# Optimization experiments

Measured on AMD Instinct MI355X. Metric: run time of the kernel, lower is better.

## Reference

```python
import jax, jax.numpy as jnp
import numpy as np

LATENT = 292
T = 120          # max_length
CHARSET = 35     # charset_length
B = 512
H1, H2, H3 = 701, 701, 901


def _p(key, shape, scale=0.05):
    return jax.random.normal(key, shape, dtype=jnp.float32) * scale


def setup_inputs() -> dict:
    key = jax.random.key(0)
    ks = jax.random.split(key, 12)
    z32 = lambda *s: jnp.zeros(s, jnp.float32)
    return {
        "z": jax.random.normal(ks[0], (B, LATENT), dtype=jnp.float32),
        # linear_1: Dense(latent_dim, selu)
        "W1": _p(ks[1], (LATENT, LATENT)), "b1": z32(LATENT),
        # gru_1 (Keras GRU, reset_after=True): kernel [in,3H], recurrent [H,3H], two bias vectors [3H]
        "gWi1": _p(ks[2], (LATENT, 3 * H1)), "gWh1": _p(ks[3], (H1, 3 * H1)),
        "gbi1": z32(3 * H1), "gbh1": z32(3 * H1),
        # gru_2
        "gWi2": _p(ks[4], (H1, 3 * H2)), "gWh2": _p(ks[5], (H2, 3 * H2)),
        "gbi2": z32(3 * H2), "gbh2": z32(3 * H2),
        # gru_3
        "gWi3": _p(ks[6], (H2, 3 * H3)), "gWh3": _p(ks[7], (H3, 3 * H3)),
        "gbi3": z32(3 * H3), "gbh3": z32(3 * H3),
        # linear_2: TimeDistributed(Dense(charset_length))
        "Wo": _p(ks[8], (H3, CHARSET)), "bo": z32(CHARSET),
    }


def _gru(x_seq, Wi, Wh, bi, bh):
    """Keras GRU (reset_after=True, gate order z,r,h), return_sequences=True.
    x_seq: [B,T,D] -> [B,T,H]. Input projections hoisted out of the scan."""
    H = Wh.shape[0]
    bsz = x_seq.shape[0]
    xp = jnp.einsum('btd,dg->btg', x_seq, Wi) + bi  # [B,T,3H]
    xp = jnp.transpose(xp, (1, 0, 2))               # [T,B,3H] for scan
    h0 = jnp.zeros((bsz, H), x_seq.dtype)

    def step(h, xt):
        rp = h @ Wh + bh                             # recurrent projection [B,3H]
        xz, xr, xh = jnp.split(xt, 3, axis=-1)
        rz, rr, rh = jnp.split(rp, 3, axis=-1)
        zg = jax.nn.sigmoid(xz + rz)
        rg = jax.nn.sigmoid(xr + rr)
        hh = jnp.tanh(xh + rg * rh)                  # reset applied after recurrent matmul
        hn = zg * h + (1.0 - zg) * hh
        return hn, hn

    _, ys = jax.lax.scan(step, h0, xp)               # ys: [T,B,H]
    return jnp.transpose(ys, (1, 0, 2))


def reference(z, W1, b1, gWi1, gWh1, gbi1, gbh1, gWi2, gWh2, gbi2, gbh2,
              gWi3, gWh3, gbi3, gbh3, Wo, bo):
    x = jax.nn.selu(z @ W1 + b1)                             # [B,latent]
    xs = jnp.broadcast_to(x[:, None, :], (x.shape[0], T, x.shape[1]))  # RepeatVector
    h = _gru(xs, gWi1, gWh1, gbi1, gbh1)                     # [B,T,701]
    h = _gru(h, gWi2, gWh2, gbi2, gbh2)                      # [B,T,701] (dropout inactive at inference)
    h = _gru(h, gWi3, gWh3, gbi3, gbh3)                      # [B,T,901]
    logits = jnp.einsum('bth,hc->btc', h, Wo) + bo           # [B,T,charset]
    return jax.nn.softmax(logits, axis=2)
```

## Files before the change

kernel.cpp:

```cpp
#include <hip/hip_runtime.h>
#include <hip/hip_bf16.h>
#include <math.h>

typedef unsigned short u16;
typedef __attribute__((ext_vector_type(4))) float f32x4;
typedef __attribute__((ext_vector_type(8))) short s16x8;

#define BB  512
#define TT  120
#define LAT 292
#define HH1 701
#define HH3 901
#define H1P 704
#define H3P 960
#define CH  35

static const size_t O_X    = 0;
static const size_t O_XP1  = 598016;
static const size_t O_H1F  = 4923392;
static const size_t O_H2F  = 7806976;
static const size_t O_H3F  = 10690560;
static const size_t O_H1B  = 14622720;
static const size_t O_H2B  = 16064512;
static const size_t O_H3B  = 17506304;
static const size_t O_WHT1 = 19472384;
static const size_t O_WIT2 = 22446080;
static const size_t O_WHT2 = 25419776;
static const size_t O_WIT3 = 28393472;
static const size_t O_WHT3 = 32358400;
static const size_t O_WOT  = 37765120;
static const size_t O_TAB  = 37888000;
static const size_t ZERO_BYTES = 14548992;

#define DSWZ(row, g) ((((g) ^ ((row) & 7)) << 4))

static __device__ __forceinline__ u16 f2b(float f){
  union { float f; unsigned int i; } v; v.f = f;
  unsigned int x = v.i;
  return (u16)((x + 0x7FFFu + ((x >> 16) & 1u)) >> 16);
}

#define GLL16(g, l) __builtin_amdgcn_global_load_lds( \
    (const __attribute__((address_space(1))) unsigned int*)(g), \
    (__attribute__((address_space(3))) unsigned int*)(l), 16, 0, 0)

__launch_bounds__(256)
__global__ void k_selu(const float* __restrict__ z, const float* __restrict__ W1,
                       const float* __restrict__ b1, float* __restrict__ x)
{
  int idx = blockIdx.x * 256 + threadIdx.x;
  if (idx >= BB * LAT) return;
  int b = idx / LAT, i = idx - b * LAT;
  float acc = b1[i];
  const float* zr = z + (size_t)b * LAT;
  for (int k = 0; k < LAT; ++k)
    acc += zr[k] * W1[k * LAT + i];
  const float alpha = 1.6732632423543772f, scale = 1.0507009873554805f;
  x[idx] = scale * (acc > 0.f ? acc : alpha * (expf(acc) - 1.f));
}

__launch_bounds__(256)
__global__ void k_xp1(const float* __restrict__ x, const float* __restrict__ Wi1,
                      const float* __restrict__ bi1, float* __restrict__ xp1)
{
  int nb = blockIdx.x % 9, bb = blockIdx.x / 9;
  int n = nb * 256 + threadIdx.x;
  int b0 = bb * 8;
  if (n >= 2112) return;
  if (n >= 2103) { for (int r = 0; r < 8; ++r) xp1[(size_t)(b0 + r) * 2112 + n] = 0.f; return; }
  float bias = bi1[n];
  float acc[8];
  for (int r = 0; r < 8; ++r) acc[r] = bias;
  for (int k = 0; k < LAT; ++k) {
    float w = Wi1[(size_t)k * 2103 + n];
    #pragma unroll
    for (int r = 0; r < 8; ++r) acc[r] += x[(size_t)(b0 + r) * LAT + k] * w;
  }
  for (int r = 0; r < 8; ++r) xp1[(size_t)(b0 + r) * 2112 + n] = acc[r];
}

__launch_bounds__(256)
__global__ void k_transpose(const float* __restrict__ W, u16* __restrict__ WT,
                            int K, int N, int Kpad, int RowsPad)
{
  int tilesN = RowsPad / 64;
  int tk = blockIdx.x / tilesN, tn = blockIdx.x % tilesN;
  int k0 = tk * 64, n0 = tn * 64;
  __shared__ u16 lds[64][72];
  int tid = threadIdx.x;
  int nl = tid & 63, q = tid >> 6;
  for (int i = 0; i < 16; ++i) {
    int kl = q * 16 + i;
    int k = k0 + kl, n = n0 + nl;
    lds[kl][nl] = (k < K && n < N) ? f2b(W[(size_t)k * N + n]) : (u16)0;
  }
  __syncthreads();
  for (int i = 0; i < 16; ++i) {
    int rl = q * 16 + i;
    WT[(size_t)(n0 + rl) * Kpad + k0 + nl] = lds[nl][rl];
  }
}

__global__ void k_maketab(unsigned int* __restrict__ tab)
{
  if (threadIdx.x != 0 || blockIdx.x != 0) return;
  for (int x = 0; x < 8; ++x) {
    for (int li = 0; li < 32; ++li) {
      unsigned v;
      if (li < 15) {
        int t3 = 15 * x + li;
        v = 0xFFFF0000u | (2u << 12) | ((unsigned)(t3 & 7) << 8) | (unsigned)(t3 >> 3);
      } else if (li < 26) {
        int t2 = 11 * x + (li - 15);
        v = 0xFFFF0000u | (1u << 12) | ((unsigned)(t2 & 7) << 8) | (unsigned)(t2 >> 3);
      } else if (li < 31) {
        int pi = 5 * x + (li - 26);
        int i0 = 2 * pi, i1 = 2 * pi + 1;
        unsigned lo = ((unsigned)(i0 & 7) << 8) | (unsigned)(i0 >> 3);
        unsigned hw = ((unsigned)(i1 & 7) << 8) | (unsigned)(i1 >> 3);
        v = lo | (hw << 16);
      } else {
        if (x < 4) {
          unsigned lo = (3u << 12) | ((unsigned)(2 * x) << 8);
          unsigned hw = (3u << 12) | ((unsigned)(2 * x + 1) << 8);
          v = lo | (hw << 16);
        } else {
          int pi = 40 + (x - 4);
          int i0 = 2 * pi, i1 = 2 * pi + 1;
          unsigned lo = ((unsigned)(i0 & 7) << 8) | (unsigned)(i0 >> 3);
          unsigned hw = ((unsigned)(i1 & 7) << 8) | (unsigned)(i1 >> 3);
          v = lo | (hw << 16);
        }
      }
      tab[x + 8 * li] = v;
    }
  }
}

#define RD32(base, row, q) ((base) + (row) * 64 + ((((q) - ((row) >> 2)) & 3) << 4))

static __device__ __forceinline__ void stage32(
    const u16* __restrict__ A, int As, const u16* __restrict__ W, int Ws, int WH,
    int r0, int j0, int kbase, int wl, int lane, char* buf)
{
  #pragma unroll
  for (int i = 0; i < 4; ++i) {
    const int si = wl * 4 + i;
    char* l = buf + si * 1024;
    if (si < 4) {
      int slot = si * 64 + lane;
      int row = slot >> 2, gl = slot & 3;
      int gq = (gl + (row >> 2)) & 3;
      GLL16(A + (size_t)(r0 + row) * As + kbase + gq * 8, l);
    } else {
      int s2 = si * 64 + lane - 256;
      int gate = s2 >> 8, loc = s2 & 255;
      int col = loc >> 2, gl = loc & 3;
      int gq = (gl + (col >> 2)) & 3;
      GLL16(W + ((size_t)gate * WH + j0 + col) * Ws + kbase + gq * 8, l);
    }
  }
}

template<int HACC>
static __device__ __forceinline__ void mm32(const char* gb, int wr, int wc, int m16, int kg,
                                            f32x4 (&acc)[4][2][2])
{
  s16x8 af[2];
  #pragma unroll
  for (int fm = 0; fm < 2; ++fm) {
    int row = wr * 32 + fm * 16 + m16;
    af[fm] = *(const s16x8*)RD32(gb, row, kg);
  }
  #pragma unroll
  for (int g = 0; g < 3; ++g) {
    #pragma unroll
    for (int fn = 0; fn < 2; ++fn) {
      int col = wc * 32 + fn * 16 + m16;
      s16x8 bf = *(const s16x8*)RD32(gb + 4096 + g * 4096, col, kg);
      const int ai = (g == 2) ? HACC : g;
      #pragma unroll
      for (int fm = 0; fm < 2; ++fm)
        acc[ai][fm][fn] = __builtin_amdgcn_mfma_f32_16x16x32_bf16(af[fm], bf, acc[ai][fm][fn], 0, 0, 0);
    }
  }
}

static __device__ __forceinline__ void gru_pipe32(
    const u16* A0, int As0, const u16* W0, int Ws0,
    const u16* A1, int As1, const u16* W1p, int Ws1,
    int WH, int n0, int n1, int k1off,
    int r0, int j0, char* ring, int wl, int lane,
    int wr, int wc, int m16, int kg, f32x4 (&acc)[4][2][2])
{
  const int n = n0 + n1;
#define STG32(C) do { int c_ = (C); char* b_ = ring + (c_ & 3) * 16384; \
    if (c_ < n0) stage32(A0, As0, W0, Ws0, WH, r0, j0, c_ * 32, wl, lane, b_); \
    else         stage32(A1, As1, W1p, Ws1, WH, r0, j0, (c_ - n0) * 32 + k1off, wl, lane, b_); \
  } while (0)
  STG32(0); STG32(1); STG32(2);
  for (int ch = 0; ch < n; ++ch) {
    if (ch + 2 < n)      asm volatile("s_waitcnt vmcnt(8)" ::: "memory");
    else if (ch + 1 < n) asm volatile("s_waitcnt vmcnt(4)" ::: "memory");
    else                 asm volatile("s_waitcnt vmcnt(0)" ::: "memory");
    __builtin_amdgcn_s_barrier();
    if (ch + 3 < n) STG32(ch + 3);
    if (ch < n0) mm32<2>(ring + (ch & 3) * 16384, wr, wc, m16, kg, acc);
    else         mm32<3>(ring + (ch & 3) * 16384, wr, wc, m16, kg, acc);
  }
#undef STG32
}

__launch_bounds__(512, 2)
__global__ void k_wave(int s, const unsigned int* __restrict__ tab,
    const u16* __restrict__ WhT1, const u16* __restrict__ WiT2, const u16* __restrict__ WhT2,
    const u16* __restrict__ WiT3, const u16* __restrict__ WhT3, const u16* __restrict__ WoT,
    const float* __restrict__ xp1,
    const float* __restrict__ gbh1,
    const float* __restrict__ gbi2, const float* __restrict__ gbh2,
    const float* __restrict__ gbi3, const float* __restrict__ gbh3,
    const float* __restrict__ bo,
    float* __restrict__ h1f, u16* __restrict__ h1b,
    float* __restrict__ h2f, u16* __restrict__ h2b,
    float* __restrict__ h3f, u16* __restrict__ h3b,
    float* __restrict__ out)
{
  extern __shared__ __align__(16) char smem[];
  const int tid  = threadIdx.x;
  const int wgrp = tid >> 8;
  const int ltid = tid & 255;
  const int lane = tid & 63;
  const int wl   = (tid >> 6) & 3;
  const int wr = wl >> 1, wc = wl & 1;
  const int m16 = lane & 15, kg = lane >> 4;
  char* ring = smem + wgrp * 65536;

  const unsigned e  = tab[blockIdx.x];
  const unsigned lo = e & 0xFFFFu, hi = e >> 16;
  const bool ksplit = (hi == 0xFFFFu);
  const unsigned item = (!ksplit && wgrp == 1) ? hi : lo;
  const int L  = (item >> 12) & 3;
  const int rr = (item >> 8) & 0xF;
  const int cc = item & 0xFF;
  const int t = s - L;
  if (t < 0 || t >= TT) return;
  const int cur = s & 1, prv = cur ^ 1;

  if (L == 3) {
    char* g0 = ring;
    const int r0 = rr * 64;
    const u16* Ab = h3b + (size_t)prv * BB * H3P;
    f32x4 acc2[2][2];
    { f32x4 z4 = {0.f,0.f,0.f,0.f}; for (int a=0;a<2;++a) for (int b=0;b<2;++b) acc2[a][b]=z4; }
    int4 ra[2], rb2[2];
    const int n = H3P / 64;
    #pragma unroll
    for (int it = 0; it < 2; ++it) {
      int gi = it * 256 + ltid; int r = gi >> 3, gq = gi & 7;
      ra[it]  = *(const int4*)(Ab + (size_t)(r0 + r) * H3P + gq * 8);
      rb2[it] = *(const int4*)(WoT + (size_t)r * H3P + gq * 8);
    }
    #pragma unroll
    for (int it = 0; it < 2; ++it) {
      int gi = it * 256 + ltid; int r = gi >> 3, gq = gi & 7;
      *(int4*)(g0 + r * 128 + DSWZ(r, gq)) = ra[it];
      *(int4*)(g0 + 8192 + r * 128 + DSWZ(r, gq)) = rb2[it];
    }
    __syncthreads();
    for (int ch = 0; ch < n; ++ch) {
      const bool have = (ch + 1 < n);
      if (have) {
        int kb = (ch + 1) * 64;
        #pragma unroll
        for (int it = 0; it < 2; ++it) {
          int gi = it * 256 + ltid; int r = gi >> 3, gq = gi & 7;
          ra[it]  = *(const int4*)(Ab + (size_t)(r0 + r) * H3P + kb + gq * 8);
          rb2[it] = *(const int4*)(WoT + (size_t)r * H3P + kb + gq * 8);
        }
      }
      #pragma unroll
      for (int s2 = 0; s2 < 2; ++s2) {
        s16x8 af[2], bf[2];
        #pragma unroll
        for (int fm = 0; fm < 2; ++fm) {
          int row = wr * 32 + fm * 16 + m16;
          af[fm] = *(const s16x8*)(g0 + row * 128 + DSWZ(row, s2 * 4 + kg));
        }
        #pragma unroll
        for (int fn = 0; fn < 2; ++fn) {
          int col = wc * 32 + fn * 16 + m16;
          bf[fn] = *(const s16x8*)(g0 + 8192 + col * 128 + DSWZ(col, s2 * 4 + kg));
        }
        #pragma unroll
        for (int fm = 0; fm < 2; ++fm)
          #pragma unroll
          for (int fn = 0; fn < 2; ++fn)
            acc2[fm][fn] = __builtin_amdgcn_mfma_f32_16x16x32_bf16(af[fm], bf[fn], acc2[fm][fn], 0, 0, 0);
      }
      if (have) {
        __syncthreads();
        #pragma unroll
        for (int it = 0; it < 2; ++it) {
          int gi = it * 256 + ltid; int r = gi >> 3, gq = gi & 7;
          *(int4*)(g0 + r * 128 + DSWZ(r, gq)) = ra[it];
          *(int4*)(g0 + 8192 + r * 128 + DSWZ(r, gq)) = rb2[it];
        }
        __syncthreads();
      }
    }
    __syncthreads();
    float (*ldsL)[68] = (float (*)[68])g0;
    #pragma unroll
    for (int fn = 0; fn < 2; ++fn) {
      int col = wc * 32 + fn * 16 + m16;
      float bov = (col < CH) ? bo[col] : 0.f;
      #pragma unroll
      for (int fm = 0; fm < 2; ++fm)
        #pragma unroll
        for (int ii = 0; ii < 4; ++ii)
          ldsL[wr * 32 + fm * 16 + kg * 4 + ii][col] = acc2[fm][fn][ii] + bov;
    }
    __syncthreads();
    if (ltid < 64) {
      int b = r0 + ltid;
      float mx = -1e30f;
      for (int c2 = 0; c2 < CH; ++c2) mx = fmaxf(mx, ldsL[ltid][c2]);
      float sum = 0.f;
      for (int c2 = 0; c2 < CH; ++c2) sum += expf(ldsL[ltid][c2] - mx);
      float inv = 1.f / sum;
      size_t ob = ((size_t)b * TT + t) * CH;
      for (int c2 = 0; c2 < CH; ++c2) out[ob + c2] = expf(ldsL[ltid][c2] - mx) * inv;
    }
    return;
  }

  int H, HP;
  const u16 *A0 = nullptr, *W0 = nullptr, *A1 = nullptr, *W1p = nullptr;
  int As0 = 0, Ws0 = 0, As1 = 0, Ws1 = 0, n0 = 0, n1 = 0, k1off = 0;
  const float *bi = nullptr, *bh;
  float *hfP, *hfC; u16 *hbC;
  if (L == 0) {
    H = HH1; HP = H1P;
    A1 = h1b + (size_t)prv * BB * H1P; As1 = H1P; W1p = WhT1; Ws1 = H1P; n1 = 22;
    bh = gbh1;
    hfP = h1f + (size_t)prv * BB * H1P; hfC = h1f + (size_t)cur * BB * H1P;
    hbC = h1b + (size_t)cur * BB * H1P;
  } else if (L == 1) {
    H = HH1; HP = H1P;
    bi = gbi2; bh = gbh2;
    hfP = h2f + (size_t)prv * BB * H1P; hfC = h2f + (size_t)cur * BB * H1P;
    hbC = h2b + (size_t)cur * BB * H1P;
    if (wgrp == 0) { A0 = h1b + (size_t)prv * BB * H1P; As0 = H1P; W0 = WiT2; Ws0 = H1P; n0 = 22; }
    else           { A1 = h2b + (size_t)prv * BB * H1P; As1 = H1P; W1p = WhT2; Ws1 = H1P; n1 = 22; }
  } else {
    H = HH3; HP = H3P;
    bi = gbi3; bh = gbh3;
    hfP = h3f + (size_t)prv * BB * H3P; hfC = h3f + (size_t)cur * BB * H3P;
    hbC = h3b + (size_t)cur * BB * H3P;
    if (wgrp == 0) {
      A0 = h2b + (size_t)prv * BB * H1P; As0 = H1P; W0 = WiT3; Ws0 = H1P; n0 = 22;
      A1 = h3b + (size_t)prv * BB * H3P; As1 = H3P; W1p = WhT3; Ws1 = H3P; n1 = 4; k1off = 0;
    } else {
      A1 = h3b + (size_t)prv * BB * H3P; As1 = H3P; W1p = WhT3; Ws1 = H3P; n1 = 26; k1off = 128;
    }
  }
  const int r0 = rr * 64, j0 = cc * 64;

  f32x4 acc[4][2][2];
  {
    f32x4 z4 = {0.f, 0.f, 0.f, 0.f};
    for (int g = 0; g < 4; ++g) for (int a = 0; a < 2; ++a) for (int b = 0; b < 2; ++b) acc[g][a][b] = z4;
  }

  gru_pipe32(A0, As0, W0, Ws0, A1, As1, W1p, Ws1, H, n0, n1, k1off,
             r0, j0, ring, wl, lane, wr, wc, m16, kg, acc);

  if (ksplit) {
    __syncthreads();
    float* red = (float*)smem;
    if (wgrp == 1) {
      float* b = red + ltid * 64;
      #pragma unroll
      for (int g = 0; g < 4; ++g)
        #pragma unroll
        for (int fm = 0; fm < 2; ++fm)
          #pragma unroll
          for (int fn = 0; fn < 2; ++fn)
            *(f32x4*)(b + ((g * 2 + fm) * 2 + fn) * 4) = acc[g][fm][fn];
    }
    __syncthreads();
    if (wgrp == 1) return;
    {
      const float* b = red + ltid * 64;
      #pragma unroll
      for (int g = 0; g < 4; ++g)
        #pragma unroll
        for (int fm = 0; fm < 2; ++fm)
          #pragma unroll
          for (int fn = 0; fn < 2; ++fn)
            acc[g][fm][fn] += *(const f32x4*)(b + ((g * 2 + fm) * 2 + fn) * 4);
    }
  }

  #pragma unroll
  for (int fn = 0; fn < 2; ++fn) {
    int j = j0 + wc * 32 + fn * 16 + m16;
    if (j >= H) continue;
    float bhz = bh[j], bhr = bh[H + j], bhh = bh[2 * H + j];
    float biz = 0.f, bir = 0.f, bih = 0.f;
    if (L != 0) { biz = bi[j]; bir = bi[H + j]; bih = bi[2 * H + j]; }
    #pragma unroll
    for (int fm = 0; fm < 2; ++fm) {
      #pragma unroll
      for (int ii = 0; ii < 4; ++ii) {
        int row = r0 + wr * 32 + fm * 16 + kg * 4 + ii;
        float az  = acc[0][fm][fn][ii];
        float ar  = acc[1][fm][fn][ii];
        float axh = acc[2][fm][fn][ii];
        float arh = acc[3][fm][fn][ii];
        float pz, pr, xh_, rh_;
        if (L == 0) {
          const float* xr_ = xp1 + (size_t)row * 2112;
          pz  = xr_[j] + az + bhz;
          pr  = xr_[HH1 + j] + ar + bhr;
          xh_ = xr_[2 * HH1 + j];
          rh_ = arh + bhh;
        } else {
          pz  = az + biz + bhz;
          pr  = ar + bir + bhr;
          xh_ = axh + bih;
          rh_ = arh + bhh;
        }
        float zg = 1.f / (1.f + expf(-pz));
        float rg = 1.f / (1.f + expf(-pr));
        float hh = tanhf(xh_ + rg * rh_);
        float hp = hfP[(size_t)row * HP + j];
        float hn = zg * hp + (1.f - zg) * hh;
        hfC[(size_t)row * HP + j] = hn;
        hbC[(size_t)row * HP + j] = f2b(hn);
      }
    }
  }
}

extern "C" void kernel_launch(void* const* d_in, const int* in_sizes, int n_in,
                              void* d_out, int out_size, void* d_ws, size_t ws_size,
                              hipStream_t stream)
{
  const float* z    = (const float*)d_in[0];
  const float* W1   = (const float*)d_in[1];
  const float* b1   = (const float*)d_in[2];
  const float* gWi1 = (const float*)d_in[3];
  const float* gWh1 = (const float*)d_in[4];
  const float* gbi1 = (const float*)d_in[5];
  const float* gbh1 = (const float*)d_in[6];
  const float* gWi2 = (const float*)d_in[7];
  const float* gWh2 = (const float*)d_in[8];
  const float* gbi2 = (const float*)d_in[9];
  const float* gbh2 = (const float*)d_in[10];
  const float* gWi3 = (const float*)d_in[11];
  const float* gWh3 = (const float*)d_in[12];
  const float* gbi3 = (const float*)d_in[13];
  const float* gbh3 = (const float*)d_in[14];
  const float* Wo   = (const float*)d_in[15];
  const float* bo   = (const float*)d_in[16];

  char* ws = (char*)d_ws;
  float* x_f  = (float*)(ws + O_X);
  float* xp1  = (float*)(ws + O_XP1);
  float* h1f  = (float*)(ws + O_H1F);
  float* h2f  = (float*)(ws + O_H2F);
  float* h3f  = (float*)(ws + O_H3F);
  u16*   h1b  = (u16*)(ws + O_H1B);
  u16*   h2b  = (u16*)(ws + O_H2B);
  u16*   h3b  = (u16*)(ws + O_H3B);
  u16*   WhT1 = (u16*)(ws + O_WHT1);
  u16*   WiT2 = (u16*)(ws + O_WIT2);
  u16*   WhT2 = (u16*)(ws + O_WHT2);
  u16*   WiT3 = (u16*)(ws + O_WIT3);
  u16*   WhT3 = (u16*)(ws + O_WHT3);
  u16*   WoT  = (u16*)(ws + O_WOT);
  unsigned int* tab = (unsigned int*)(ws + O_TAB);

  hipFuncSetAttribute((const void*)k_wave,
                      hipFuncAttributeMaxDynamicSharedMemorySize, 131072);

  hipMemsetAsync(ws + O_H1F, 0, ZERO_BYTES, stream);

  k_maketab<<<1, 64, 0, stream>>>(tab);
  k_selu<<<(BB * LAT + 255) / 256, 256, 0, stream>>>(z, W1, b1, x_f);
  k_xp1<<<9 * 64, 256, 0, stream>>>(x_f, gWi1, gbi1, xp1);

  k_transpose<<<11 * 33, 256, 0, stream>>>(gWh1, WhT1, 701, 2103, 704, 2112);
  k_transpose<<<11 * 33, 256, 0, stream>>>(gWi2, WiT2, 701, 2103, 704, 2112);
  k_transpose<<<11 * 33, 256, 0, stream>>>(gWh2, WhT2, 701, 2103, 704, 2112);
  k_transpose<<<11 * 44, 256, 0, stream>>>(gWi3, WiT3, 701, 2703, 704, 2816);
  k_transpose<<<15 * 44, 256, 0, stream>>>(gWh3, WhT3, 901, 2703, 960, 2816);
  k_transpose<<<15 * 1, 256, 0, stream>>>(Wo, WoT, 901, 35, 960, 64);

  for (int s = 0; s < TT + 3; ++s)
    k_wave<<<256, 512, 131072, stream>>>(s, tab, WhT1, WiT2, WhT2, WiT3, WhT3, WoT, xp1,
                                         gbh1, gbi2, gbh2, gbi3, gbh3, bo,
                                         h1f, h1b, h2f, h2b, h3f, h3b, (float*)d_out);
}
```

Measured before the change: 5.001 ms.

## Fuse per-step wave launches into one persistent kernel with grid barrier

Replaces the 123 per-timestep k_wave launches with a single persistent k_all kernel. The blocks synchronise through an atomic counter grid barrier after each step and pad with dummy __syncthreads so every block issues the same barrier count. The previous hidden state now stays in registers, which removes the fp32 h buffers and their global reads and writes. The bf16 state is written with cache-bypassing stores and read through LDS loads with coherence bits, and the output layer now uses the same async LDS pipeline. This removes launch overhead and global traffic, but it relies on all 256 blocks being co-resident, and the spin barrier has a timeout guard that could break correctness if the guard fires.

```diff
diff --git a/kernel.cpp b/kernel.cpp
--- a/kernel.cpp
+++ b/kernel.cpp
@@ -14,12 +14,11 @@
 #define H1P 704
 #define H3P 960
 #define CH  35
+#define NSTEP (TT + 3)
+#define STEP_BARS 32
 
 static const size_t O_X    = 0;
 static const size_t O_XP1  = 598016;
-static const size_t O_H1F  = 4923392;
-static const size_t O_H2F  = 7806976;
-static const size_t O_H3F  = 10690560;
 static const size_t O_H1B  = 14622720;
 static const size_t O_H2B  = 16064512;
 static const size_t O_H3B  = 17506304;
@@ -30,9 +29,8 @@
 static const size_t O_WHT3 = 32358400;
 static const size_t O_WOT  = 37765120;
 static const size_t O_TAB  = 37888000;
-static const size_t ZERO_BYTES = 14548992;
-
-#define DSWZ(row, g) ((((g) ^ ((row) & 7)) << 4))
+static const size_t O_CNT  = 37889024;
+static const size_t ZERO_HB = 4849664;
 
 static __device__ __forceinline__ u16 f2b(float f){
   union { float f; unsigned int i; } v; v.f = f;
@@ -40,9 +38,16 @@
   return (u16)((x + 0x7FFFu + ((x >> 16) & 1u)) >> 16);
 }
 
-#define GLL16(g, l) __builtin_amdgcn_global_load_lds( \
+#define GLLB(g, l) __builtin_amdgcn_global_load_lds( \
     (const __attribute__((address_space(1))) unsigned int*)(g), \
     (__attribute__((address_space(3))) unsigned int*)(l), 16, 0, 0)
+#define GLLA(g, l) __builtin_amdgcn_global_load_lds( \
+    (const __attribute__((address_space(1))) unsigned int*)(g), \
+    (__attribute__((address_space(3))) unsigned int*)(l), 16, 0, 17)
+
+static __device__ __forceinline__ void st_u16_sc(u16* p, u16 v) {
+  asm volatile("global_store_short %0, %1, off sc0 sc1" :: "v"(p), "v"((unsigned)v) : "memory");
+}
 
 __launch_bounds__(256)
 __global__ void k_selu(const float* __restrict__ z, const float* __restrict__ W1,
@@ -151,14 +156,32 @@
       int slot = si * 64 + lane;
       int row = slot >> 2, gl = slot & 3;
       int gq = (gl + (row >> 2)) & 3;
-      GLL16(A + (size_t)(r0 + row) * As + kbase + gq * 8, l);
+      GLLA(A + (size_t)(r0 + row) * As + kbase + gq * 8, l);
     } else {
       int s2 = si * 64 + lane - 256;
       int gate = s2 >> 8, loc = s2 & 255;
       int col = loc >> 2, gl = loc & 3;
       int gq = (gl + (col >> 2)) & 3;
-      GLL16(W + ((size_t)gate * WH + j0 + col) * Ws + kbase + gq * 8, l);
+      GLLB(W + ((size_t)gate * WH + j0 + col) * Ws + kbase + gq * 8, l);
     }
+  }
+}
+
+static __device__ __forceinline__ void stage_out(
+    const u16* __restrict__ A, const u16* __restrict__ Wo,
+    int r0, int kbase, int wl, int lane, char* buf)
+{
+  {
+    int slot = wl * 64 + lane;
+    int row = slot >> 2, gl = slot & 3;
+    int gq = (gl + (row >> 2)) & 3;
+    GLLA(A + (size_t)(r0 + row) * H3P + kbase + gq * 8, buf + wl * 1024);
+  }
+  {
+    int slot = wl * 64 + lane;
+    int col = slot >> 2, gl = slot & 3;
+    int gq = (gl + (col >> 2)) & 3;
+    GLLB(Wo + (size_t)col * H3P + kbase + gq * 8, buf + 4096 + wl * 1024);
   }
 }
 
@@ -184,6 +207,27 @@
         acc[ai][fm][fn] = __builtin_amdgcn_mfma_f32_16x16x32_bf16(af[fm], bf, acc[ai][fm][fn], 0, 0, 0);
     }
   }
+}
+
+static __device__ __forceinline__ void mm_out(const char* gb, int wr, int wc, int m16, int kg,
+                                              f32x4 (&acc2)[2][2])
+{
+  s16x8 af[2], bf[2];
+  #pragma unroll
+  for (int fm = 0; fm < 2; ++fm) {
+    int row = wr * 32 + fm * 16 + m16;
+    af[fm] = *(const s16x8*)RD32(gb, row, kg);
+  }
+  #pragma unroll
+  for (int fn = 0; fn < 2; ++fn) {
+    int col = wc * 32 + fn * 16 + m16;
+    bf[fn] = *(const s16x8*)RD32(gb + 4096, col, kg);
+  }
+  #pragma unroll
+  for (int fm = 0; fm < 2; ++fm)
+    #pragma unroll
+    for (int fn = 0; fn < 2; ++fn)
+      acc2[fm][fn] = __builtin_amdgcn_mfma_f32_16x16x32_bf16(af[fm], bf[fn], acc2[fm][fn], 0, 0, 0);
 }
 
 static __device__ __forceinline__ void gru_pipe32(
@@ -212,7 +256,7 @@
 }
 
 __launch_bounds__(512, 2)
-__global__ void k_wave(int s, const unsigned int* __restrict__ tab,
+__global__ void k_all(const unsigned int* __restrict__ tab, unsigned int* __restrict__ cnt,
     const u16* __restrict__ WhT1, const u16* __restrict__ WiT2, const u16* __restrict__ WhT2,
     const u16* __restrict__ WiT3, const u16* __restrict__ WhT3, const u16* __restrict__ WoT,
     const float* __restrict__ xp1,
@@ -220,9 +264,7 @@
     const float* __restrict__ gbi2, const float* __restrict__ gbh2,
     const float* __restrict__ gbi3, const float* __restrict__ gbh3,
     const float* __restrict__ bo,
-    float* __restrict__ h1f, u16* __restrict__ h1b,
-    float* __restrict__ h2f, u16* __restrict__ h2b,
-    float* __restrict__ h3f, u16* __restrict__ h3b,
+    u16* __restrict__ h1b, u16* __restrict__ h2b, u16* __restrict__ h3b,
     float* __restrict__ out)
 {
   extern __shared__ __align__(16) char smem[];
@@ -242,204 +284,178 @@
   const int L  = (item >> 12) & 3;
   const int rr = (item >> 8) & 0xF;
   const int cc = item & 0xFF;
-  const int t = s - L;
-  if (t < 0 || t >= TT) return;
-  const int cur = s & 1, prv = cur ^ 1;
-
-  if (L == 3) {
-    char* g0 = ring;
-    const int r0 = rr * 64;
-    const u16* Ab = h3b + (size_t)prv * BB * H3P;
-    f32x4 acc2[2][2];
-    { f32x4 z4 = {0.f,0.f,0.f,0.f}; for (int a=0;a<2;++a) for (int b=0;b<2;++b) acc2[a][b]=z4; }
-    int4 ra[2], rb2[2];
-    const int n = H3P / 64;
-    #pragma unroll
-    for (int it = 0; it < 2; ++it) {
-      int gi = it * 256 + ltid; int r = gi >> 3, gq = gi & 7;
-      ra[it]  = *(const int4*)(Ab + (size_t)(r0 + r) * H3P + gq * 8);
-      rb2[it] = *(const int4*)(WoT + (size_t)r * H3P + gq * 8);
+  const int r0 = rr * 64, j0 = cc * 64;
+
+  int H = 0, As0 = 0, Ws0 = 0, As1 = 0, Ws1 = 0, n0 = 0, n1 = 0, k1off = 0;
+  const u16 *A0base = nullptr, *W0p = nullptr, *A1base = nullptr, *W1p = nullptr;
+  u16 *hbCbase = nullptr;
+  const float *bi = nullptr, *bh = nullptr;
+  bool do_epi = true;
+  if (L == 0) {
+    H = HH1;
+    A1base = h1b; As1 = H1P; W1p = WhT1; Ws1 = H1P; n1 = 22;
+    bh = gbh1; hbCbase = h1b;
+  } else if (L == 1) {
+    H = HH1; bi = gbi2; bh = gbh2; hbCbase = h2b;
+    if (wgrp == 0) { A0base = h1b; As0 = H1P; W0p = WiT2; Ws0 = H1P; n0 = 22; As1 = H1P; }
+    else           { A1base = h2b; As1 = H1P; W1p = WhT2; Ws1 = H1P; n1 = 22; }
+    do_epi = (wgrp == 0);
+  } else if (L == 2) {
+    H = HH3; bi = gbi3; bh = gbh3; hbCbase = h3b;
+    if (wgrp == 0) {
+      A0base = h2b; As0 = H1P; W0p = WiT3; Ws0 = H1P; n0 = 22;
+      A1base = h3b; As1 = H3P; W1p = WhT3; Ws1 = H3P; n1 = 4; k1off = 0;
+    } else {
+      A1base = h3b; As1 = H3P; W1p = WhT3; Ws1 = H3P; n1 = 26; k1off = 128;
     }
-    #pragma unroll
-    for (int it = 0; it < 2; ++it) {
-      int gi = it * 256 + ltid; int r = gi >> 3, gq = gi & 7;
-      *(int4*)(g0 + r * 128 + DSWZ(r, gq)) = ra[it];
-      *(int4*)(g0 + 8192 + r * 128 + DSWZ(r, gq)) = rb2[it];
-    }
-    __syncthreads();
-    for (int ch = 0; ch < n; ++ch) {
-      const bool have = (ch + 1 < n);
-      if (have) {
-        int kb = (ch + 1) * 64;
-        #pragma unroll
-        for (int it = 0; it < 2; ++it) {
-          int gi = it * 256 + ltid; int r = gi >> 3, gq = gi & 7;
-          ra[it]  = *(const int4*)(Ab + (size_t)(r0 + r) * H3P + kb + gq * 8);
-          rb2[it] = *(const int4*)(WoT + (size_t)r * H3P + kb + gq * 8);
+    do_epi = (wgrp == 0);
+  }
+
+  f32x4 hp_[2][2];
+  { f32x4 z4 = {0.f,0.f,0.f,0.f}; for (int a=0;a<2;++a) for (int b=0;b<2;++b) hp_[a][b]=z4; }
+
+  for (int s = 0; s < NSTEP; ++s) {
+    const int t = s - L;
+    const int cur = s & 1, prv = cur ^ 1;
+    int used = 0;
+
+    if (t >= 0 && t < TT) {
+      if (L == 3) {
+        const u16* Ab = h3b + (size_t)prv * BB * H3P;
+        f32x4 acc2[2][2];
+        { f32x4 z4 = {0.f,0.f,0.f,0.f}; for (int a=0;a<2;++a) for (int b=0;b<2;++b) acc2[a][b]=z4; }
+        const int n = H3P / 32;
+        stage_out(Ab, WoT, r0, 0, wl, lane, ring);
+        stage_out(Ab, WoT, r0, 32, wl, lane, ring + 8192);
+        stage_out(Ab, WoT, r0, 64, wl, lane, ring + 16384);
+        for (int ch = 0; ch < n; ++ch) {
+          if (ch + 2 < n)      asm volatile("s_waitcnt vmcnt(4)" ::: "memory");
+          else if (ch + 1 < n) asm volatile("s_waitcnt vmcnt(2)" ::: "memory");
+          else                 asm volatile("s_waitcnt vmcnt(0)" ::: "memory");
+          __builtin_amdgcn_s_barrier();
+          if (ch + 3 < n) stage_out(Ab, WoT, r0, (ch + 3) * 32, wl, lane, ring + ((ch + 3) & 3) * 8192);
+          mm_out(ring + (ch & 3) * 8192, wr, wc, m16, kg, acc2);
         }
-      }
-      #pragma unroll
-      for (int s2 = 0; s2 < 2; ++s2) {
-        s16x8 af[2], bf[2];
-        #pragma unroll
-        for (int fm = 0; fm < 2; ++fm) {
-          int row = wr * 32 + fm * 16 + m16;
-          af[fm] = *(const s16x8*)(g0 + row * 128 + DSWZ(row, s2 * 4 + kg));
-        }
+        __syncthreads();
+        float (*ldsL)[68] = (float (*)[68])ring;
         #pragma unroll
         for (int fn = 0; fn < 2; ++fn) {
           int col = wc * 32 + fn * 16 + m16;
-          bf[fn] = *(const s16x8*)(g0 + 8192 + col * 128 + DSWZ(col, s2 * 4 + kg));
-        }
-        #pragma unroll
-        for (int fm = 0; fm < 2; ++fm)
+          float bov = (col < CH) ? bo[col] : 0.f;
           #pragma unroll
-          for (int fn = 0; fn < 2; ++fn)
-            acc2[fm][fn] = __builtin_amdgcn_mfma_f32_16x16x32_bf16(af[fm], bf[fn], acc2[fm][fn], 0, 0, 0);
-      }
-      if (have) {
-        __syncthreads();
-        #pragma unroll
-        for (int it = 0; it < 2; ++it) {
-          int gi = it * 256 + ltid; int r = gi >> 3, gq = gi & 7;
-          *(int4*)(g0 + r * 128 + DSWZ(r, gq)) = ra[it];
-          *(int4*)(g0 + 8192 + r * 128 + DSWZ(r, gq)) = rb2[it];
+          for (int fm = 0; fm < 2; ++fm)
+            #pragma unroll
+            for (int ii = 0; ii < 4; ++ii)
+              ldsL[wr * 32 + fm * 16 + kg * 4 + ii][col] = acc2[fm][fn][ii] + bov;
         }
         __syncthreads();
+        if (ltid < 64) {
+          int b = r0 + ltid;
+          float mx = -1e30f;
+          for (int c2 = 0; c2 < CH; ++c2) mx = fmaxf(mx, ldsL[ltid][c2]);
+          float sum = 0.f;
+          for (int c2 = 0; c2 < CH; ++c2) sum += expf(ldsL[ltid][c2] - mx);
+          float inv = 1.f / sum;
+          size_t ob = ((size_t)b * TT + t) * CH;
+          for (int c2 = 0; c2 < CH; ++c2) out[ob + c2] = expf(ldsL[ltid][c2] - mx) * inv;
+        }
+        used = STEP_BARS;
+      } else {
+        const u16* A0 = A0base ? A0base + (size_t)prv * BB * As0 : nullptr;
+        const u16* A1 = A1base ? A1base + (size_t)prv * BB * As1 : nullptr;
+        u16* hbC = hbCbase + (size_t)cur * BB * As1;
+
+        f32x4 acc[4][2][2];
+        { f32x4 z4 = {0.f,0.f,0.f,0.f};
+          for (int g = 0; g < 4; ++g) for (int a = 0; a < 2; ++a) for (int b = 0; b < 2; ++b) acc[g][a][b] = z4; }
+
+        gru_pipe32(A0, As0, W0p, Ws0, A1, As1, W1p, Ws1, H, n0, n1, k1off,
+                   r0, j0, ring, wl, lane, wr, wc, m16, kg, acc);
+        used = n0 + n1;
+
+        if (ksplit) {
+          __syncthreads();
+          float* red = (float*)smem;
+          if (wgrp == 1) {
+            float* b = red + ltid * 64;
+            #pragma unroll
+            for (int g = 0; g < 4; ++g)
+              #pragma unroll
+              for (int fm = 0; fm < 2; ++fm)
+                #pragma unroll
+                for (int fn = 0; fn < 2; ++fn)
+                  *(f32x4*)(b + ((g * 2 + fm) * 2 + fn) * 4) = acc[g][fm][fn];
+          }
+          __syncthreads();
+          used += 2;
+          if (wgrp == 0) {
+            const float* b = red + ltid * 64;
+            #pragma unroll
+            for (int g = 0; g < 4; ++g)
+              #pragma unroll
+              for (int fm = 0; fm < 2; ++fm)
+                #pragma unroll
+                for (int fn = 0; fn < 2; ++fn)
+                  acc[g][fm][fn] += *(const f32x4*)(b + ((g * 2 + fm) * 2 + fn) * 4);
+          }
+        }
+
+        if (do_epi) {
+          #pragma unroll
+          for (int fn = 0; fn < 2; ++fn) {
+            int j = j0 + wc * 32 + fn * 16 + m16;
+            if (j >= H) continue;
+            float bhz = bh[j], bhr = bh[H + j], bhh = bh[2 * H + j];
+            float biz = 0.f, bir = 0.f, bih = 0.f;
+            if (L != 0) { biz = bi[j]; bir = bi[H + j]; bih = bi[2 * H + j]; }
+            #pragma unroll
+            for (int fm = 0; fm < 2; ++fm) {
+              #pragma unroll
+              for (int ii = 0; ii < 4; ++ii) {
+                int row = r0 + wr * 32 + fm * 16 + kg * 4 + ii;
+                float az  = acc[0][fm][fn][ii];
+                float ar  = acc[1][fm][fn][ii];
+                float axh = acc[2][fm][fn][ii];
+                float arh = acc[3][fm][fn][ii];
+                float pz, pr, xh_, rh_;
+                if (L == 0) {
+                  const float* xr_ = xp1 + (size_t)row * 2112;
+                  pz  = xr_[j] + az + bhz;
+                  pr  = xr_[HH1 + j] + ar + bhr;
+                  xh_ = xr_[2 * HH1 + j];
+                  rh_ = arh + bhh;
+                } else {
+                  pz  = az + biz + bhz;
+                  pr  = ar + bir + bhr;
+                  xh_ = axh + bih;
+                  rh_ = arh + bhh;
+                }
+                float zg = 1.f / (1.f + expf(-pz));
+                float rg = 1.f / (1.f + expf(-pr));
+                float hh = tanhf(xh_ + rg * rh_);
+                float hn = zg * hp_[fn][fm][ii] + (1.f - zg) * hh;
+                hp_[fn][fm][ii] = hn;
+                st_u16_sc(&hbC[(size_t)row * As1 + j], f2b(hn));
+              }
+            }
+          }
+        }
+      }
+    }
+
+    for (int k = used; k < STEP_BARS; ++k) __syncthreads();
+
+    asm volatile("s_waitcnt vmcnt(0)" ::: "memory");
+    __syncthreads();
+    if (tid == 0) {
+      atomicAdd(&cnt[s], 1u);
+      int guard = 0;
+      while (__hip_atomic_load(&cnt[s], __ATOMIC_RELAXED, __HIP_MEMORY_SCOPE_AGENT) < 256u) {
+        __builtin_amdgcn_s_sleep(2);
+        if (++guard > (1 << 18)) break;
       }
     }
     __syncthreads();
-    float (*ldsL)[68] = (float (*)[68])g0;
-    #pragma unroll
-    for (int fn = 0; fn < 2; ++fn) {
-      int col = wc * 32 + fn * 16 + m16;
-      float bov = (col < CH) ? bo[col] : 0.f;
-      #pragma unroll
-      for (int fm = 0; fm < 2; ++fm)
-        #pragma unroll
-        for (int ii = 0; ii < 4; ++ii)
-          ldsL[wr * 32 + fm * 16 + kg * 4 + ii][col] = acc2[fm][fn][ii] + bov;
-    }
-    __syncthreads();
-    if (ltid < 64) {
-      int b = r0 + ltid;
-      float mx = -1e30f;
-      for (int c2 = 0; c2 < CH; ++c2) mx = fmaxf(mx, ldsL[ltid][c2]);
-      float sum = 0.f;
-      for (int c2 = 0; c2 < CH; ++c2) sum += expf(ldsL[ltid][c2] - mx);
-      float inv = 1.f / sum;
-      size_t ob = ((size_t)b * TT + t) * CH;
-      for (int c2 = 0; c2 < CH; ++c2) out[ob + c2] = expf(ldsL[ltid][c2] - mx) * inv;
-    }
-    return;
-  }
-
-  int H, HP;
-  const u16 *A0 = nullptr, *W0 = nullptr, *A1 = nullptr, *W1p = nullptr;
-  int As0 = 0, Ws0 = 0, As1 = 0, Ws1 = 0, n0 = 0, n1 = 0, k1off = 0;
-  const float *bi = nullptr, *bh;
-  float *hfP, *hfC; u16 *hbC;
-  if (L == 0) {
-    H = HH1; HP = H1P;
-    A1 = h1b + (size_t)prv * BB * H1P; As1 = H1P; W1p = WhT1; Ws1 = H1P; n1 = 22;
-    bh = gbh1;
-    hfP = h1f + (size_t)prv * BB * H1P; hfC = h1f + (size_t)cur * BB * H1P;
-    hbC = h1b + (size_t)cur * BB * H1P;
-  } else if (L == 1) {
-    H = HH1; HP = H1P;
-    bi = gbi2; bh = gbh2;
-    hfP = h2f + (size_t)prv * BB * H1P; hfC = h2f + (size_t)cur * BB * H1P;
-    hbC = h2b + (size_t)cur * BB * H1P;
-    if (wgrp == 0) { A0 = h1b + (size_t)prv * BB * H1P; As0 = H1P; W0 = WiT2; Ws0 = H1P; n0 = 22; }
-    else           { A1 = h2b + (size_t)prv * BB * H1P; As1 = H1P; W1p = WhT2; Ws1 = H1P; n1 = 22; }
-  } else {
-    H = HH3; HP = H3P;
-    bi = gbi3; bh = gbh3;
-    hfP = h3f + (size_t)prv * BB * H3P; hfC = h3f + (size_t)cur * BB * H3P;
-    hbC = h3b + (size_t)cur * BB * H3P;
-    if (wgrp == 0) {
-      A0 = h2b + (size_t)prv * BB * H1P; As0 = H1P; W0 = WiT3; Ws0 = H1P; n0 = 22;
-      A1 = h3b + (size_t)prv * BB * H3P; As1 = H3P; W1p = WhT3; Ws1 = H3P; n1 = 4; k1off = 0;
-    } else {
-      A1 = h3b + (size_t)prv * BB * H3P; As1 = H3P; W1p = WhT3; Ws1 = H3P; n1 = 26; k1off = 128;
-    }
-  }
-  const int r0 = rr * 64, j0 = cc * 64;
-
-  f32x4 acc[4][2][2];
-  {
-    f32x4 z4 = {0.f, 0.f, 0.f, 0.f};
-    for (int g = 0; g < 4; ++g) for (int a = 0; a < 2; ++a) for (int b = 0; b < 2; ++b) acc[g][a][b] = z4;
-  }
-
-  gru_pipe32(A0, As0, W0, Ws0, A1, As1, W1p, Ws1, H, n0, n1, k1off,
-             r0, j0, ring, wl, lane, wr, wc, m16, kg, acc);
-
-  if (ksplit) {
-    __syncthreads();
-    float* red = (float*)smem;
-    if (wgrp == 1) {
-      float* b = red + ltid * 64;
-      #pragma unroll
-      for (int g = 0; g < 4; ++g)
-        #pragma unroll
-        for (int fm = 0; fm < 2; ++fm)
-          #pragma unroll
-          for (int fn = 0; fn < 2; ++fn)
-            *(f32x4*)(b + ((g * 2 + fm) * 2 + fn) * 4) = acc[g][fm][fn];
-    }
-    __syncthreads();
-    if (wgrp == 1) return;
-    {
-      const float* b = red + ltid * 64;
-      #pragma unroll
-      for (int g = 0; g < 4; ++g)
-        #pragma unroll
-        for (int fm = 0; fm < 2; ++fm)
-          #pragma unroll
-          for (int fn = 0; fn < 2; ++fn)
-            acc[g][fm][fn] += *(const f32x4*)(b + ((g * 2 + fm) * 2 + fn) * 4);
-    }
-  }
-
-  #pragma unroll
-  for (int fn = 0; fn < 2; ++fn) {
-    int j = j0 + wc * 32 + fn * 16 + m16;
-    if (j >= H) continue;
-    float bhz = bh[j], bhr = bh[H + j], bhh = bh[2 * H + j];
-    float biz = 0.f, bir = 0.f, bih = 0.f;
-    if (L != 0) { biz = bi[j]; bir = bi[H + j]; bih = bi[2 * H + j]; }
-    #pragma unroll
-    for (int fm = 0; fm < 2; ++fm) {
-      #pragma unroll
-      for (int ii = 0; ii < 4; ++ii) {
-        int row = r0 + wr * 32 + fm * 16 + kg * 4 + ii;
-        float az  = acc[0][fm][fn][ii];
-        float ar  = acc[1][fm][fn][ii];
-        float axh = acc[2][fm][fn][ii];
-        float arh = acc[3][fm][fn][ii];
-        float pz, pr, xh_, rh_;
-        if (L == 0) {
-          const float* xr_ = xp1 + (size_t)row * 2112;
-          pz  = xr_[j] + az + bhz;
-          pr  = xr_[HH1 + j] + ar + bhr;
-          xh_ = xr_[2 * HH1 + j];
-          rh_ = arh + bhh;
-        } else {
-          pz  = az + biz + bhz;
-          pr  = ar + bir + bhr;
-          xh_ = axh + bih;
-          rh_ = arh + bhh;
-        }
-        float zg = 1.f / (1.f + expf(-pz));
-        float rg = 1.f / (1.f + expf(-pr));
-        float hh = tanhf(xh_ + rg * rh_);
-        float hp = hfP[(size_t)row * HP + j];
-        float hn = zg * hp + (1.f - zg) * hh;
-        hfC[(size_t)row * HP + j] = hn;
-        hbC[(size_t)row * HP + j] = f2b(hn);
-      }
-    }
   }
 }
 
@@ -468,9 +484,6 @@
   char* ws = (char*)d_ws;
   float* x_f  = (float*)(ws + O_X);
   float* xp1  = (float*)(ws + O_XP1);
-  float* h1f  = (float*)(ws + O_H1F);
-  float* h2f  = (float*)(ws + O_H2F);
-  float* h3f  = (float*)(ws + O_H3F);
   u16*   h1b  = (u16*)(ws + O_H1B);
   u16*   h2b  = (u16*)(ws + O_H2B);
   u16*   h3b  = (u16*)(ws + O_H3B);
@@ -481,11 +494,13 @@
   u16*   WhT3 = (u16*)(ws + O_WHT3);
   u16*   WoT  = (u16*)(ws + O_WOT);
   unsigned int* tab = (unsigned int*)(ws + O_TAB);
-
-  hipFuncSetAttribute((const void*)k_wave,
+  unsigned int* cnt = (unsigned int*)(ws + O_CNT);
+
+  hipFuncSetAttribute((const void*)k_all,
                       hipFuncAttributeMaxDynamicSharedMemorySize, 131072);
 
-  hipMemsetAsync(ws + O_H1F, 0, ZERO_BYTES, stream);
+  hipMemsetAsync(ws + O_H1B, 0, ZERO_HB, stream);
+  hipMemsetAsync(ws + O_CNT, 0, NSTEP * 4, stream);
 
   k_maketab<<<1, 64, 0, stream>>>(tab);
   k_selu<<<(BB * LAT + 255) / 256, 256, 0, stream>>>(z, W1, b1, x_f);
@@ -498,8 +513,7 @@
   k_transpose<<<15 * 44, 256, 0, stream>>>(gWh3, WhT3, 901, 2703, 960, 2816);
   k_transpose<<<15 * 1, 256, 0, stream>>>(Wo, WoT, 901, 35, 960, 64);
 
-  for (int s = 0; s < TT + 3; ++s)
-    k_wave<<<256, 512, 131072, stream>>>(s, tab, WhT1, WiT2, WhT2, WiT3, WhT3, WoT, xp1,
-                                         gbh1, gbi2, gbh2, gbi3, gbh3, bo,
-                                         h1f, h1b, h2f, h2b, h3f, h3b, (float*)d_out);
-}
+  k_all<<<256, 512, 131072, stream>>>(tab, cnt, WhT1, WiT2, WhT2, WiT3, WhT3, WoT, xp1,
+                                      gbh1, gbi2, gbh2, gbi3, gbh3, bo,
+                                      h1b, h2b, h3b, (float*)d_out);
+}
```

Measured after the change: 6.997 ms. +39.9%, slower.
